# Optimization experiments

Hardware: AMD Instinct MI355X
Metric: run time of the kernel (lower is better)

Reference implementation:

```python
import jax, jax.numpy as jnp
import numpy as np

N_NODES = 8192   # Hopfield neurons == Kuramoto oscillators
D_OSC = 64       # oscillator vector dimension
E_K = 1048576    # Kuramoto-Kuramoto edges
E_HK = 1048576   # Hopfield-Kuramoto coupling edges


def setup_inputs() -> dict:
    key = jax.random.key(0)
    ks = jax.random.split(key, 8)
    state_H = jax.random.normal(ks[0], (N_NODES,), dtype=jnp.float32)
    state_K = jax.random.normal(ks[1], (N_NODES, D_OSC), dtype=jnp.float32)
    ind_K = jax.random.randint(ks[2], (E_K, 2), 0, N_NODES, dtype=jnp.int32)
    ind_HK = jax.random.randint(ks[3], (E_HK, 2), 0, N_NODES, dtype=jnp.int32)
    weights_H = jax.random.normal(ks[4], (N_NODES, N_NODES), dtype=jnp.float32) / np.sqrt(N_NODES).astype(np.float32)
    bias_H = jax.random.normal(ks[5], (N_NODES,), dtype=jnp.float32) / np.sqrt(N_NODES).astype(np.float32)
    weights_HK = jax.random.normal(ks[6], (E_HK, 1), dtype=jnp.float32)
    w_K = jax.random.normal(ks[7], (E_K,), dtype=jnp.float32)
    kappa_K = jnp.ones((1,), dtype=jnp.float32)
    kappa_H = jnp.ones((1,), dtype=jnp.float32)
    return {"state_H": state_H, "state_K": state_K, "ind_K": ind_K, "ind_HK": ind_HK,
            "kappa_K": kappa_K, "kappa_H": kappa_H, "weights_H": weights_H,
            "bias_H": bias_H, "weights_HK": weights_HK, "w_K": w_K}


def reference(state_H, state_K, ind_K, ind_HK, kappa_K, kappa_H,
              weights_H, bias_H, weights_HK, w_K):
    # normalize oscillator states to unit sphere
    state_K = state_K / jnp.linalg.norm(state_K, axis=1, keepdims=True)
    # Lagrangian net: L = sum log cosh  ->  g = tanh
    g = jnp.tanh(state_H)                                  # [N]

    i0, i1 = ind_HK[:, 0], ind_HK[:, 1]
    w_hk = weights_HK[:, 0]                                # [E_HK]
    Gram = jnp.sum(state_K[i0] * state_K[i1], axis=1)      # [E_HK]

    f_H = jnp.zeros_like(g)
    f_H = f_H.at[i0].add(Gram * w_hk * g[i1] / kappa_H)
    f_H = f_H.at[i1].add(Gram * w_hk * g[i0] / kappa_H)
    f_H = f_H + (weights_H + weights_H.T) @ g / 2 - state_H + bias_H

    j0, j1 = ind_K[:, 0], ind_K[:, 1]
    s = jnp.sum(state_K[j0] * state_K[j1], axis=1)          # [E_K]
    # interaction_K: per-edge linear coupling, dE/ds = w_K * s
    dE_ds = (w_K * s)[:, None]                              # [E_K,1]

    f_K = jnp.zeros_like(state_K)
    f_K = f_K.at[j0].add(dE_ds * state_K[j1])
    f_K = f_K.at[j1].add(dE_ds * state_K[j0])

    G = (g[i0] * g[i1])[:, None]                            # [E_HK,1]
    f_K = f_K.at[i0].add(-G * weights_HK * state_K[i1] / kappa_K)
    f_K = f_K.at[i1].add(-G * weights_HK * state_K[i0] / kappa_K)

    # project dynamics onto tangent space of the sphere
    f_K = -f_K + state_K * jnp.sum(state_K * f_K, axis=1, keepdims=True)
    return (f_H, f_K)
```

## Files before the change

### kernel.cpp

```cpp
#include <hip/hip_runtime.h>
#include <cstdint>

#define N_NODES 8192
#define D_OSC   64
#define E_EDGE  1048576

__device__ __forceinline__ float waveReduceSum(float v) {
#pragma unroll
  for (int off = 32; off > 0; off >>= 1)
    v += __shfl_xor(v, off, 64);
  return v;
}

__global__ void k_prep_scalar(const float* __restrict__ sH, float* g, float* y1,
                              float* y2, int* cnt) {
  int i = blockIdx.x * blockDim.x + threadIdx.x;
  if (i < N_NODES) {
    g[i] = tanhf(sH[i]);
    y1[i] = 0.f;
    y2[i] = 0.f;
    cnt[i] = 0;
  }
}

__global__ void k_normalize(const float* __restrict__ stateK, float* __restrict__ sK) {
  int node = blockIdx.x * (blockDim.x >> 6) + (threadIdx.x >> 6);
  int lane = threadIdx.x & 63;
  float v = stateK[node * D_OSC + lane];
  float ss = waveReduceSum(v * v);
  sK[node * D_OSC + lane] = v / sqrtf(ss);
}

__global__ void k_count(const int2* __restrict__ indK, const int2* __restrict__ indHK,
                        int* cnt) {
  int stride = gridDim.x * blockDim.x;
  for (int idx = blockIdx.x * blockDim.x + threadIdx.x; idx < 2 * E_EDGE; idx += stride) {
    int2 pr = (idx < E_EDGE) ? indK[idx] : indHK[idx - E_EDGE];
    atomicAdd(&cnt[pr.x], 1);
    atomicAdd(&cnt[pr.y], 1);
  }
}

__global__ void k_scan(const int* __restrict__ cnt, int* offs, int* curs) {
  __shared__ int lds[256];
  int t = threadIdx.x;
  int local[32];
  int s = 0;
#pragma unroll
  for (int k = 0; k < 32; ++k) { local[k] = cnt[t * 32 + k]; s += local[k]; }
  lds[t] = s;
  __syncthreads();
  for (int off = 1; off < 256; off <<= 1) {
    int v = (t >= off) ? lds[t - off] : 0;
    __syncthreads();
    lds[t] += v;
    __syncthreads();
  }
  int run = lds[t] - s;
#pragma unroll
  for (int k = 0; k < 32; ++k) {
    offs[t * 32 + k] = run;
    curs[t * 32 + k] = run;
    run += local[k];
  }
  if (t == 255) offs[N_NODES] = run;
}

__global__ void k_coeff_fill(const float* __restrict__ sK, const int2* __restrict__ indK,
                             const int2* __restrict__ indHK, const float* __restrict__ wK,
                             const float* __restrict__ wHK, const float* __restrict__ g,
                             const float* __restrict__ kH, const float* __restrict__ kK,
                             int* curs, int4* __restrict__ recs) {
  int lane = threadIdx.x & 63;
  int grp = lane >> 4;
  int l16 = lane & 15;
  int wid = (blockIdx.x * blockDim.x + threadIdx.x) >> 6;
  int nw = (gridDim.x * blockDim.x) >> 6;
  float rKH = 1.f / kH[0];
  float rKK = 1.f / kK[0];
  const float4* sK4 = (const float4*)sK;
  for (int base = wid * 4; base < 2 * E_EDGE; base += nw * 4) {
    int w = base + grp;
    int set = w >= E_EDGE;
    int e = set ? w - E_EDGE : w;
    int2 pr = set ? indHK[e] : indK[e];
    float4 a = sK4[pr.x * 16 + l16];
    float4 b = sK4[pr.y * 16 + l16];
    float d = a.x * b.x + a.y * b.y + a.z * b.z + a.w * b.w;
#pragma unroll
    for (int off = 8; off > 0; off >>= 1) d += __shfl_xor(d, off, 64);
    if (l16 == 0) {
      float cf, hx, hy;
      if (set) {
        float ww = wHK[e];
        float ch = d * ww * rKH;
        float gx = g[pr.x], gy = g[pr.y];
        cf = -gx * gy * ww * rKK;
        hx = ch * gy;
        hy = ch * gx;
      } else {
        cf = wK[e] * d;
        hx = 0.f;
        hy = 0.f;
      }
      int p0 = atomicAdd(&curs[pr.x], 1);
      recs[p0] = make_int4(pr.y, __float_as_int(cf), __float_as_int(hx), 0);
      int p1 = atomicAdd(&curs[pr.y], 1);
      recs[p1] = make_int4(pr.x, __float_as_int(cf), __float_as_int(hy), 0);
    }
  }
}

#define MV_ROWS 32
#define MV_CB   2048
__global__ __launch_bounds__(256) void k_matvec(const float* __restrict__ W,
                                                const float* __restrict__ g,
                                                float* y1, float* y2) {
  int t = threadIdx.x;
  int r0 = blockIdx.x * MV_ROWS;
  int c0 = blockIdx.y * MV_CB;
  int wid = t >> 6, lane = t & 63;
  float gcol[8], y2p[8];
#pragma unroll
  for (int k = 0; k < 8; ++k) { gcol[k] = g[c0 + t + 256 * k]; y2p[k] = 0.f; }
  __shared__ float red[MV_ROWS][4];
  for (int r = 0; r < MV_ROWS; ++r) {
    int i = r0 + r;
    float gi = g[i];
    const float* row = W + (size_t)i * N_NODES + c0 + t;
    float acc = 0.f;
#pragma unroll
    for (int k = 0; k < 8; ++k) {
      float w = row[256 * k];
      acc = fmaf(w, gcol[k], acc);
      y2p[k] = fmaf(w, gi, y2p[k]);
    }
    acc = waveReduceSum(acc);
    if (lane == 0) red[r][wid] = acc;
  }
  __syncthreads();
  if (t < MV_ROWS)
    atomicAdd(&y1[r0 + t], red[t][0] + red[t][1] + red[t][2] + red[t][3]);
#pragma unroll
  for (int k = 0; k < 8; ++k) atomicAdd(&y2[c0 + t + 256 * k], y2p[k]);
}

__global__ void k_gather(const float* __restrict__ sK, const int* __restrict__ offs,
                         const int4* __restrict__ recs, const float* __restrict__ y1,
                         const float* __restrict__ y2, const float* __restrict__ sH,
                         const float* __restrict__ bias, float* __restrict__ out) {
  int node = blockIdx.x * (blockDim.x >> 6) + (threadIdx.x >> 6);
  int lane = threadIdx.x & 63;
  float skl = sK[node * D_OSC + lane];
  int beg = __builtin_amdgcn_readfirstlane(offs[node]);
  int end = __builtin_amdgcn_readfirstlane(offs[node + 1]);
  float acc = 0.f, accH = 0.f;
  int p = beg;
  for (; p + 8 <= end; p += 8) {
    int4 r[8];
#pragma unroll
    for (int j = 0; j < 8; ++j) r[j] = recs[p + j];
    float v[8];
#pragma unroll
    for (int j = 0; j < 8; ++j) v[j] = sK[r[j].x * D_OSC + lane];
#pragma unroll
    for (int j = 0; j < 8; ++j) {
      acc = fmaf(__int_as_float(r[j].y), v[j], acc);
      accH += __int_as_float(r[j].z);
    }
  }
  for (; p < end; ++p) {
    int4 r0 = recs[p];
    acc = fmaf(__int_as_float(r0.y), sK[r0.x * D_OSC + lane], acc);
    accH += __int_as_float(r0.z);
  }
  float dot = waveReduceSum(skl * acc);
  out[N_NODES + node * D_OSC + lane] = fmaf(skl, dot, -acc);
  if (lane == 0)
    out[node] = accH + 0.5f * (y1[node] + y2[node]) - sH[node] + bias[node];
}

extern "C" void kernel_launch(void* const* d_in, const int* in_sizes, int n_in,
                              void* d_out, int out_size, void* d_ws, size_t ws_size,
                              hipStream_t stream) {
  const float* state_H    = (const float*)d_in[0];
  const float* state_K    = (const float*)d_in[1];
  const int2*  ind_K      = (const int2*)d_in[2];
  const int2*  ind_HK     = (const int2*)d_in[3];
  const float* kappa_K    = (const float*)d_in[4];
  const float* kappa_H    = (const float*)d_in[5];
  const float* weights_H  = (const float*)d_in[6];
  const float* bias_H     = (const float*)d_in[7];
  const float* weights_HK = (const float*)d_in[8];
  const float* w_K        = (const float*)d_in[9];
  float* out = (float*)d_out;

  char* w = (char*)d_ws;
  float* sK   = (float*)w; w += (size_t)N_NODES * D_OSC * 4;
  float* g    = (float*)w; w += (size_t)N_NODES * 4;
  float* y1   = (float*)w; w += (size_t)N_NODES * 4;
  float* y2   = (float*)w; w += (size_t)N_NODES * 4;
  int*   cnt  = (int*)w;   w += (size_t)N_NODES * 4;
  int*   offs = (int*)w;   w += (size_t)(N_NODES + 16) * 4;
  int*   curs = (int*)w;   w += (size_t)N_NODES * 4;
  int4*  recs = (int4*)w;

  k_prep_scalar<<<N_NODES / 256, 256, 0, stream>>>(state_H, g, y1, y2, cnt);
  k_normalize<<<N_NODES / 4, 256, 0, stream>>>(state_K, sK);
  k_count<<<2048, 256, 0, stream>>>(ind_K, ind_HK, cnt);
  k_scan<<<1, 256, 0, stream>>>(cnt, offs, curs);
  k_coeff_fill<<<4096, 256, 0, stream>>>(sK, ind_K, ind_HK, w_K, weights_HK, g,
                                         kappa_H, kappa_K, curs, recs);
  k_matvec<<<dim3(N_NODES / MV_ROWS, N_NODES / MV_CB), 256, 0, stream>>>(weights_H, g,
                                                                         y1, y2);
  k_gather<<<N_NODES / 4, 256, 0, stream>>>(sK, offs, recs, y1, y2, state_H, bias_H,
                                            out);
}
```

Measured before the change: 840.8 us.

## Replace per-node CSR build with bucketed LDS-staged scatter and shared-memory gather

```diff
diff --git a/kernel.cpp b/kernel.cpp
--- a/kernel.cpp
+++ b/kernel.cpp
@@ -4,6 +4,10 @@
 #define N_NODES 8192
 #define D_OSC   64
 #define E_EDGE  1048576
+#define NBUCKET 512
+#define NPB     16
+#define BCAP    12288
+#define CHUNK   2048
 
 __device__ __forceinline__ float waveReduceSum(float v) {
 #pragma unroll
@@ -12,15 +16,16 @@
   return v;
 }
 
-__global__ void k_prep_scalar(const float* __restrict__ sH, float* g, float* y1,
-                              float* y2, int* cnt) {
+__global__ void k_prep(const float* __restrict__ sH, float* g, float* y1, float* y2,
+                       float* fH, int* cursor) {
   int i = blockIdx.x * blockDim.x + threadIdx.x;
   if (i < N_NODES) {
     g[i] = tanhf(sH[i]);
     y1[i] = 0.f;
     y2[i] = 0.f;
-    cnt[i] = 0;
-  }
+    fH[i] = 0.f;
+  }
+  if (i < NBUCKET) cursor[i] = 0;
 }
 
 __global__ void k_normalize(const float* __restrict__ stateK, float* __restrict__ sK) {
@@ -31,83 +36,67 @@
   sK[node * D_OSC + lane] = v / sqrtf(ss);
 }
 
-__global__ void k_count(const int2* __restrict__ indK, const int2* __restrict__ indHK,
-                        int* cnt) {
-  int stride = gridDim.x * blockDim.x;
-  for (int idx = blockIdx.x * blockDim.x + threadIdx.x; idx < 2 * E_EDGE; idx += stride) {
-    int2 pr = (idx < E_EDGE) ? indK[idx] : indHK[idx - E_EDGE];
-    atomicAdd(&cnt[pr.x], 1);
-    atomicAdd(&cnt[pr.y], 1);
-  }
-}
-
-__global__ void k_scan(const int* __restrict__ cnt, int* offs, int* curs) {
-  __shared__ int lds[256];
+__global__ __launch_bounds__(256) void k_coeff_scatter(
+    const float* __restrict__ sK, const int2* __restrict__ indK,
+    const int2* __restrict__ indHK, const float* __restrict__ wK,
+    const float* __restrict__ wHK, const float* __restrict__ g,
+    const float* __restrict__ kH, const float* __restrict__ kK,
+    int* cursor, float* fH, int2* __restrict__ recs) {
+  __shared__ int2     recS[2 * CHUNK];
+  __shared__ unsigned keyS[2 * CHUNK];
+  __shared__ int      histS[NBUCKET];
+  __shared__ int      baseS[NBUCKET];
   int t = threadIdx.x;
-  int local[32];
-  int s = 0;
-#pragma unroll
-  for (int k = 0; k < 32; ++k) { local[k] = cnt[t * 32 + k]; s += local[k]; }
-  lds[t] = s;
-  __syncthreads();
-  for (int off = 1; off < 256; off <<= 1) {
-    int v = (t >= off) ? lds[t - off] : 0;
-    __syncthreads();
-    lds[t] += v;
-    __syncthreads();
-  }
-  int run = lds[t] - s;
-#pragma unroll
-  for (int k = 0; k < 32; ++k) {
-    offs[t * 32 + k] = run;
-    curs[t * 32 + k] = run;
-    run += local[k];
-  }
-  if (t == 255) offs[N_NODES] = run;
-}
-
-__global__ void k_coeff_fill(const float* __restrict__ sK, const int2* __restrict__ indK,
-                             const int2* __restrict__ indHK, const float* __restrict__ wK,
-                             const float* __restrict__ wHK, const float* __restrict__ g,
-                             const float* __restrict__ kH, const float* __restrict__ kK,
-                             int* curs, int4* __restrict__ recs) {
-  int lane = threadIdx.x & 63;
-  int grp = lane >> 4;
-  int l16 = lane & 15;
-  int wid = (blockIdx.x * blockDim.x + threadIdx.x) >> 6;
-  int nw = (gridDim.x * blockDim.x) >> 6;
+  for (int s = t; s < NBUCKET; s += 256) histS[s] = 0;
+  __syncthreads();
+
+  int l16 = t & 15;
+  int grp = t >> 4;
+  int set = (int)(blockIdx.x >= (E_EDGE / CHUNK));
+  const int2* ind = set ? indHK : indK;
+  int e0 = blockIdx.x * CHUNK - set * E_EDGE;
   float rKH = 1.f / kH[0];
   float rKK = 1.f / kK[0];
   const float4* sK4 = (const float4*)sK;
-  for (int base = wid * 4; base < 2 * E_EDGE; base += nw * 4) {
-    int w = base + grp;
-    int set = w >= E_EDGE;
-    int e = set ? w - E_EDGE : w;
-    int2 pr = set ? indHK[e] : indK[e];
+
+  for (int i = 0; i < CHUNK / 16; ++i) {
+    int el = i * 16 + grp;
+    int e = e0 + el;
+    int2 pr = ind[e];
     float4 a = sK4[pr.x * 16 + l16];
     float4 b = sK4[pr.y * 16 + l16];
     float d = a.x * b.x + a.y * b.y + a.z * b.z + a.w * b.w;
 #pragma unroll
     for (int off = 8; off > 0; off >>= 1) d += __shfl_xor(d, off, 64);
     if (l16 == 0) {
-      float cf, hx, hy;
+      float cf;
       if (set) {
         float ww = wHK[e];
         float ch = d * ww * rKH;
         float gx = g[pr.x], gy = g[pr.y];
         cf = -gx * gy * ww * rKK;
-        hx = ch * gy;
-        hy = ch * gx;
+        unsafeAtomicAdd(&fH[pr.x], ch * gy);
+        unsafeAtomicAdd(&fH[pr.y], ch * gx);
       } else {
         cf = wK[e] * d;
-        hx = 0.f;
-        hy = 0.f;
       }
-      int p0 = atomicAdd(&curs[pr.x], 1);
-      recs[p0] = make_int4(pr.y, __float_as_int(cf), __float_as_int(hx), 0);
-      int p1 = atomicAdd(&curs[pr.y], 1);
-      recs[p1] = make_int4(pr.x, __float_as_int(cf), __float_as_int(hy), 0);
-    }
+      int bx = pr.x >> 4, by = pr.y >> 4;
+      int rx = atomicAdd(&histS[bx], 1);
+      int ry = atomicAdd(&histS[by], 1);
+      recS[2 * el]     = make_int2(pr.y | ((pr.x & (NPB - 1)) << 16), __float_as_int(cf));
+      keyS[2 * el]     = ((unsigned)bx << 16) | (unsigned)rx;
+      recS[2 * el + 1] = make_int2(pr.x | ((pr.y & (NPB - 1)) << 16), __float_as_int(cf));
+      keyS[2 * el + 1] = ((unsigned)by << 16) | (unsigned)ry;
+    }
+  }
+  __syncthreads();
+  for (int s = t; s < NBUCKET; s += 256)
+    baseS[s] = atomicAdd(&cursor[s], histS[s]);
+  __syncthreads();
+  for (int s = t; s < 2 * CHUNK; s += 256) {
+    unsigned k = keyS[s];
+    int bkt = k >> 16;
+    recs[(size_t)bkt * BCAP + baseS[bkt] + (k & 0xFFFFu)] = recS[s];
   }
 }
 
@@ -145,39 +134,58 @@
   for (int k = 0; k < 8; ++k) atomicAdd(&y2[c0 + t + 256 * k], y2p[k]);
 }
 
-__global__ void k_gather(const float* __restrict__ sK, const int* __restrict__ offs,
-                         const int4* __restrict__ recs, const float* __restrict__ y1,
-                         const float* __restrict__ y2, const float* __restrict__ sH,
-                         const float* __restrict__ bias, float* __restrict__ out) {
-  int node = blockIdx.x * (blockDim.x >> 6) + (threadIdx.x >> 6);
-  int lane = threadIdx.x & 63;
-  float skl = sK[node * D_OSC + lane];
-  int beg = __builtin_amdgcn_readfirstlane(offs[node]);
-  int end = __builtin_amdgcn_readfirstlane(offs[node + 1]);
-  float acc = 0.f, accH = 0.f;
-  int p = beg;
-  for (; p + 8 <= end; p += 8) {
-    int4 r[8];
-#pragma unroll
-    for (int j = 0; j < 8; ++j) r[j] = recs[p + j];
-    float v[8];
-#pragma unroll
-    for (int j = 0; j < 8; ++j) v[j] = sK[r[j].x * D_OSC + lane];
-#pragma unroll
-    for (int j = 0; j < 8; ++j) {
-      acc = fmaf(__int_as_float(r[j].y), v[j], acc);
-      accH += __int_as_float(r[j].z);
-    }
-  }
-  for (; p < end; ++p) {
-    int4 r0 = recs[p];
-    acc = fmaf(__int_as_float(r0.y), sK[r0.x * D_OSC + lane], acc);
-    accH += __int_as_float(r0.z);
-  }
-  float dot = waveReduceSum(skl * acc);
-  out[N_NODES + node * D_OSC + lane] = fmaf(skl, dot, -acc);
-  if (lane == 0)
-    out[node] = accH + 0.5f * (y1[node] + y2[node]) - sH[node] + bias[node];
+__global__ __launch_bounds__(512) void k_gather(
+    const float* __restrict__ sK, const int* __restrict__ cursor,
+    const int2* __restrict__ recs, const float* __restrict__ fH,
+    const float* __restrict__ y1, const float* __restrict__ y2,
+    const float* __restrict__ sH, const float* __restrict__ bias,
+    float* __restrict__ out) {
+  __shared__ float fld[NPB * D_OSC];
+  int b = blockIdx.x;
+  int t = threadIdx.x;
+  for (int s = t; s < NPB * D_OSC; s += 512) fld[s] = 0.f;
+  __syncthreads();
+  int cnt = cursor[b];
+  const int2* rb = recs + (size_t)b * BCAP;
+  int wave = t >> 6, lane = t & 63;
+
+  int ntile = cnt >> 4;
+  for (int i = wave; i < ntile; i += 8) {
+    int p0 = i << 4;
+    int2 r = rb[p0 + (lane & 15)];
+#pragma unroll
+    for (int j = 0; j < 16; ++j) {
+      int w0 = __shfl(r.x, j, 64);
+      float cf = __int_as_float(__shfl(r.y, j, 64));
+      float v = sK[(w0 & 0xFFFF) * D_OSC + lane];
+      atomicAdd(&fld[(w0 >> 16) * D_OSC + lane], cf * v);
+    }
+  }
+  if (wave == 0) {
+    int p0 = ntile << 4;
+    int tail = cnt - p0;
+    if (tail > 0) {
+      int2 r = rb[p0 + (lane & 15)];
+      for (int j = 0; j < tail; ++j) {
+        int w0 = __shfl(r.x, j, 64);
+        float cf = __int_as_float(__shfl(r.y, j, 64));
+        float v = sK[(w0 & 0xFFFF) * D_OSC + lane];
+        atomicAdd(&fld[(w0 >> 16) * D_OSC + lane], cf * v);
+      }
+    }
+  }
+  __syncthreads();
+  for (int n = wave; n < NPB; n += 8) {
+    int node = b * NPB + n;
+    float fv = fld[n * D_OSC + lane];
+    float skl = sK[node * D_OSC + lane];
+    float dot = waveReduceSum(skl * fv);
+    out[N_NODES + node * D_OSC + lane] = fmaf(skl, dot, -fv);
+  }
+  if (t < NPB) {
+    int node = b * NPB + t;
+    out[node] = fH[node] + 0.5f * (y1[node] + y2[node]) - sH[node] + bias[node];
+  }
 }
 
 extern "C" void kernel_launch(void* const* d_in, const int* in_sizes, int n_in,
@@ -200,19 +208,17 @@
   float* g    = (float*)w; w += (size_t)N_NODES * 4;
   float* y1   = (float*)w; w += (size_t)N_NODES * 4;
   float* y2   = (float*)w; w += (size_t)N_NODES * 4;
-  int*   cnt  = (int*)w;   w += (size_t)N_NODES * 4;
-  int*   offs = (int*)w;   w += (size_t)(N_NODES + 16) * 4;
-  int*   curs = (int*)w;   w += (size_t)N_NODES * 4;
-  int4*  recs = (int4*)w;
-
-  k_prep_scalar<<<N_NODES / 256, 256, 0, stream>>>(state_H, g, y1, y2, cnt);
+  float* fH   = (float*)w; w += (size_t)N_NODES * 4;
+  int*   curs = (int*)w;   w += (size_t)NBUCKET * 4;
+  w = (char*)(((uintptr_t)w + 255) & ~(uintptr_t)255);
+  int2*  recs = (int2*)w;
+
+  k_prep<<<N_NODES / 256, 256, 0, stream>>>(state_H, g, y1, y2, fH, curs);
   k_normalize<<<N_NODES / 4, 256, 0, stream>>>(state_K, sK);
-  k_count<<<2048, 256, 0, stream>>>(ind_K, ind_HK, cnt);
-  k_scan<<<1, 256, 0, stream>>>(cnt, offs, curs);
-  k_coeff_fill<<<4096, 256, 0, stream>>>(sK, ind_K, ind_HK, w_K, weights_HK, g,
-                                         kappa_H, kappa_K, curs, recs);
+  k_coeff_scatter<<<2 * E_EDGE / CHUNK, 256, 0, stream>>>(
+      sK, ind_K, ind_HK, w_K, weights_HK, g, kappa_H, kappa_K, curs, fH, recs);
   k_matvec<<<dim3(N_NODES / MV_ROWS, N_NODES / MV_CB), 256, 0, stream>>>(weights_H, g,
                                                                          y1, y2);
-  k_gather<<<N_NODES / 4, 256, 0, stream>>>(sK, offs, recs, y1, y2, state_H, bias_H,
-                                            out);
-}
+  k_gather<<<NBUCKET, 512, 0, stream>>>(sK, curs, recs, fH, y1, y2, state_H, bias_H,
+                                        out);
+}
```

Result: slower. 2.158 ms (+156.7%).
